# Kernel optimization log

Hardware: AMD Instinct MI355X
Metric: run time of the kernel (lower is better)

The kernel has to match this reference:

```python
import jax, jax.numpy as jnp
import numpy as np

H = 512      # hidden_dim
K = 3        # conv_kernel_size
CHUNK = 3    # chunk_size
EPS = 1e-5   # BatchNorm eps


def conv1d(x, w, b, pad):
    # x: (B, Cin, L), w: (Cout, Cin, K)
    y = jax.lax.conv_general_dilated(x, w, (1,), [(pad, pad)],
                                     dimension_numbers=("NCH", "OIH", "NCH"))
    return y + b[None, :, None]


def chunk_indices(seq_lens):
    # static int metadata -> numpy index build (loop over small fixed batch only)
    sl = np.asarray(seq_lens)
    bidx, sidx = [], []
    for b, l in enumerate(sl):
        starts = np.arange(0, int(l) - CHUNK + 1, CHUNK)
        bidx.append(np.full(starts.shape[0], b, dtype=np.int32))
        sidx.append(starts.astype(np.int32))
    return np.concatenate(bidx), np.concatenate(sidx)


def setup_inputs() -> dict:
    key = jax.random.key(0)
    ks = jax.random.split(key, 8)
    B, L = 32, 4096
    x = jax.random.normal(ks[0], (B, L), jnp.float32)
    seq_lens = jax.random.randint(ks[1], (B,), 2048, L + 1)

    def w(k, shape):
        return jax.random.normal(k, shape, jnp.float32) * 0.05

    return {
        "x": x,
        "w0": w(ks[2], (H, 1, K)), "b0": jnp.zeros((H,)), "g0": jnp.ones((H,)), "be0": jnp.zeros((H,)),
        "w1": w(ks[3], (H, H, K)), "b1": jnp.zeros((H,)), "g1": jnp.ones((H,)), "be1": jnp.zeros((H,)),
        "w2": w(ks[4], (H, H, K)), "b2": jnp.zeros((H,)), "g2": jnp.ones((H,)), "be2": jnp.zeros((H,)),
        "pw": w(ks[5], (H, H, CHUNK)), "pb": jnp.zeros((H,)),
        "fw": w(ks[6], (1, H)), "fb": jnp.zeros((1,)),
        "seq_lens": seq_lens,
    }


def reference(x, w0, b0, g0, be0, w1, b1, g1, be1, w2, b2, g2, be2,
              pw, pb, fw, fb, seq_lens):
    inv = np.float32(1.0 / np.sqrt(1.0 + EPS))  # BN eval: mean=0, var=1
    h = x[:, None, :]  # (B, 1, L)
    for (w, b, g, be) in ((w0, b0, g0, be0), (w1, b1, g1, be1), (w2, b2, g2, be2)):
        h = jax.nn.relu(conv1d(h, w, b, pad=1))
        h = (g * inv)[None, :, None] * h + be[None, :, None]
    h = jnp.transpose(h, (0, 2, 1))  # (B, L, H)

    bidx_np, sidx_np = chunk_indices(seq_lens)
    bidx = jnp.asarray(bidx_np)
    sidx = jnp.asarray(sidx_np)
    offs = jnp.arange(CHUNK, dtype=jnp.int32)
    chunks = h[bidx[:, None], sidx[:, None] + offs[None, :], :]  # (N, CHUNK, H)

    # pre_fc_conv over a length-CHUNK window == one GEMM per chunk
    z = jnp.einsum("nth,cht->nc", chunks, pw) + pb  # (N, H)
    logits = jax.nn.relu(z) @ fw.T + fb             # (N, 1)
    return jax.nn.sigmoid(logits)[:, 0]             # (N,)
```

## Files before the change

### kernel.cpp

```cpp
#include <hip/hip_runtime.h>

#define HCH 512
#define LSEQ 4096
#define HSTR (LSEQ + 4)
#define NB 32
#define KW 3
#define KDIM 1536
#define SPAD 1408
#define INVS 0.9999950000374997f
#define NT 24

typedef __attribute__((ext_vector_type(8))) short bf16x8;
typedef __attribute__((ext_vector_type(4))) float f32x4;

__device__ inline unsigned short f2bf(float f) {
  unsigned int u = __float_as_uint(f);
  u += 0x7fffu + ((u >> 16) & 1u);
  return (unsigned short)(u >> 16);
}

__device__ inline void gl_lds16(const void* g, void* l) {
  __builtin_amdgcn_global_load_lds(
      (const __attribute__((address_space(1))) void*)g,
      (__attribute__((address_space(3))) void*)l, 16, 0, 0);
}

__global__ void prep_all(const float* __restrict__ w1, const float* __restrict__ w2,
                         const float* __restrict__ pw, unsigned short* __restrict__ wt,
                         const int* __restrict__ seq_lens, int* __restrict__ cum,
                         float* __restrict__ pz, int nz,
                         unsigned short* __restrict__ hbuf, int nbp) {
  int idx = blockIdx.x * 256 + threadIdx.x;
  if (idx < nz) pz[idx] = 0.f;
  if (idx == 0) {
    int acc = 0;
    for (int b = 0; b < NB; b++) {
      cum[b] = acc;
      acc += (seq_lens[b] - KW) / KW + 1;
    }
  }
  int npads = 2 * nbp * 4 * HCH;
  if (idx < npads) {
    int per = nbp * 4 * HCH;
    int buf = idx / per, r = idx % per;
    int b = r / (4 * HCH), rr = r % (4 * HCH);
    int j = rr / HCH, c = rr % HCH;
    int row = (j == 0) ? 0 : (LSEQ + j);
    hbuf[((size_t)buf * nbp + b) * HSTR * HCH + (size_t)row * HCH + c] = 0;
  }
  if (idx < 3 * HCH * KDIM) {
    int which = idx / (HCH * KDIM);
    int r = idx % (HCH * KDIM);
    int c = r / KDIM;
    int rem = r % KDIM;
    int k = rem / HCH, ci = rem % HCH;
    const float* src = (which == 0) ? w1 : ((which == 1) ? w2 : pw);
    wt[idx] = f2bf(src[c * KDIM + ci * KW + k]);
  }
}

__global__ void layer0(const float* __restrict__ x, const float* __restrict__ w0,
                       const float* __restrict__ b0, const float* __restrict__ g0,
                       const float* __restrict__ be0, unsigned short* __restrict__ h0,
                       const int* __restrict__ seq_q) {
  int tid = threadIdx.x;
  int wave = tid >> 6, lane = tid & 63;
  int pos0 = (blockIdx.x * 4 + wave) * 8;
  int l0 = pos0 & (LSEQ - 1);
  int bq = pos0 >> 12;
  if (l0 >= seq_q[bq] + 2) return;
  int c0 = lane * 8;

  float w[24], bb[8], gg[8], ee[8];
  for (int v = 0; v < 6; v++)
    *reinterpret_cast<float4*>(w + v * 4) = *reinterpret_cast<const float4*>(w0 + c0 * 3 + v * 4);
  for (int v = 0; v < 2; v++) {
    *reinterpret_cast<float4*>(bb + v * 4) = *reinterpret_cast<const float4*>(b0 + c0 + v * 4);
    *reinterpret_cast<float4*>(gg + v * 4) = *reinterpret_cast<const float4*>(g0 + c0 + v * 4);
    *reinterpret_cast<float4*>(ee + v * 4) = *reinterpret_cast<const float4*>(be0 + c0 + v * 4);
  }
  for (int c = 0; c < 8; c++) gg[c] *= INVS;

  const float* xb = x + (size_t)(pos0 - l0);
  unsigned short* hrow = h0 + ((size_t)bq * HSTR + 1 + l0) * HCH + c0;
  for (int pp = 0; pp < 8; pp++) {
    int l = l0 + pp;
    float xm1 = (l > 0) ? xb[l - 1] : 0.f;
    float xc = xb[l];
    float xp1 = (l < LSEQ - 1) ? xb[l + 1] : 0.f;
    unsigned int o[4];
    for (int pq = 0; pq < 4; pq++) {
      unsigned int lo = 0, hi = 0;
      for (int s = 0; s < 2; s++) {
        int c = pq * 2 + s;
        float y = w[c * 3] * xm1 + w[c * 3 + 1] * xc + w[c * 3 + 2] * xp1 + bb[c];
        y = fmaxf(y, 0.f);
        unsigned int u = f2bf(gg[c] * y + ee[c]);
        if (s == 0) lo = u; else hi = u;
      }
      o[pq] = lo | (hi << 16);
    }
    uint4 v4; v4.x = o[0]; v4.y = o[1]; v4.z = o[2]; v4.w = o[3];
    *reinterpret_cast<uint4*>(hrow + (size_t)pp * HCH) = v4;
  }
}

#define OFFK(T) (((T) % 3) * HCH + ((T) / 3) * 64)

#define STAGE_A(Mh, AB, TN)                                                 \
  { char* d_ = ldsc + (AB) * 32768 + (Mh) * 16384 + w * 1024;               \
    gl_lds16(aSrc[Mh][0] + OFFK(TN), d_);                                   \
    gl_lds16(aSrc[Mh][1] + OFFK(TN), d_ + 8192); }

#define STAGE_B(Nh, BB, TN)                                                 \
  { char* d_ = ldsc + 65536 + (BB) * 32768 + (Nh) * 16384 + w * 1024;       \
    gl_lds16(bSrc[Nh][0] + OFFK(TN), d_);                                   \
    gl_lds16(bSrc[Nh][1] + OFFK(TN), d_ + 8192); }

#define LOAD_AF(Mh, AB)                                                     \
  _Pragma("unroll") for (int i_ = 0; i_ < 4; ++i_)                          \
  _Pragma("unroll") for (int s_ = 0; s_ < 2; ++s_)                          \
    af[i_][s_] = *reinterpret_cast<const bf16x8*>(                          \
        ldsb + (AB) * 16384 + (Mh) * 8192 + (wm + i_ * 16 + mr) * 64 +      \
        (((s_ * 4 + quad) ^ (mr & 7)) << 3));

#define LOAD_BF(Nh, BB)                                                     \
  _Pragma("unroll") for (int j_ = 0; j_ < 2; ++j_)                          \
  _Pragma("unroll") for (int s_ = 0; s_ < 2; ++s_)                          \
    bfv[Nh][j_][s_] = *reinterpret_cast<const bf16x8*>(                     \
        ldsb + 32768 + (BB) * 16384 + (Nh) * 8192 + (wn + j_ * 16 + mr) * 64 + \
        (((s_ * 4 + quad) ^ (mr & 7)) << 3));

#define MFMA_Q(Mh, Nh)                                                      \
  __builtin_amdgcn_s_setprio(1);                                            \
  _Pragma("unroll") for (int i_ = 0; i_ < 4; ++i_)                          \
  _Pragma("unroll") for (int j_ = 0; j_ < 2; ++j_)                          \
  _Pragma("unroll") for (int s_ = 0; s_ < 2; ++s_)                          \
    acc[(Mh)*4 + i_][(Nh)*2 + j_] = __builtin_amdgcn_mfma_f32_16x16x32_bf16( \
        af[i_][s_], bfv[Nh][j_][s_], acc[(Mh)*4 + i_][(Nh)*2 + j_], 0, 0, 0); \
  __builtin_amdgcn_s_setprio(0);

#define BARRIER { asm volatile("" ::: "memory");                            \
                  __builtin_amdgcn_s_barrier();                             \
                  asm volatile("" ::: "memory"); }
#define WAITV(n) asm volatile("s_waitcnt vmcnt(" #n ")" ::: "memory");

#define STEP(T)                                                             \
  {                                                                         \
    if ((T) == NT - 1) { WAITV(0); } else { WAITV(4); }                     \
    BARRIER;                                                                \
    if ((T) + 1 < NT) { STAGE_A(0, ((T)+1)&1, (T)+1);                       \
                        STAGE_A(1, ((T)+1)&1, (T)+1); }                     \
    if ((T) + 2 < NT) { STAGE_B(0, ((T)+2)%3, (T)+2);                       \
                        STAGE_B(1, ((T)+2)%3, (T)+2); }                     \
    bf16x8 af[4][2], bfv[2][2][2];                                          \
    LOAD_AF(0, (T)&1);                                                      \
    LOAD_BF(0, (T)%3); LOAD_BF(1, (T)%3);                                   \
    MFMA_Q(0, 0); MFMA_Q(0, 1);                                             \
    LOAD_AF(1, (T)&1);                                                      \
    MFMA_Q(1, 1); MFMA_Q(1, 0);                                             \
  }

__global__ __launch_bounds__(512, 2) void conv_gemm8(
    const unsigned short* __restrict__ hin,
    const unsigned short* __restrict__ wT,
    const float* __restrict__ bconv, const float* __restrict__ g,
    const float* __restrict__ be,
    unsigned short* __restrict__ hout,
    const int* __restrict__ seq_q, int margin) {
  __shared__ unsigned short ldsb[81920];

  int f = blockIdx.x;
  int cpx = gridDim.x >> 3;
  int s = (f & 7) * cpx + (f >> 3);
  int cm = (s & 1) << 8;
  int y = s >> 1;
  int b = y >> 4;
  int l0 = (y & 15) << 8;
  int limit = seq_q[b] + margin;
  if (l0 >= limit) return;

  const size_t hb = (size_t)b * HSTR * HCH + HCH;
  int tid = threadIdx.x;
  int w = tid >> 6, lane = tid & 63;
  int quad = lane >> 4, mr = lane & 15;
  int wm = (w >> 2) << 6;
  int wn = (w & 3) << 5;
  int srow = tid >> 3;
  int sslot8 = (((tid & 7) ^ (srow & 7)) << 3);

  const unsigned short* aSrc[2][2];
#pragma unroll
  for (int Mh = 0; Mh < 2; ++Mh)
#pragma unroll
    for (int g2 = 0; g2 < 2; ++g2)
      aSrc[Mh][g2] = wT + (size_t)(cm + Mh * 128 + g2 * 64 + srow) * KDIM + sslot8;
  const unsigned short* bSrc[2][2];
#pragma unroll
  for (int Nh = 0; Nh < 2; ++Nh)
#pragma unroll
    for (int g2 = 0; g2 < 2; ++g2)
      bSrc[Nh][g2] = hin + hb +
          (size_t)(l0 - 1 + Nh * 128 + g2 * 64 + srow) * HCH + sslot8;

  f32x4 acc[8][4] = {};
  char* ldsc = (char*)ldsb;

  STAGE_A(0, 0, 0); STAGE_A(1, 0, 0);
  STAGE_B(0, 0, 0); STAGE_B(1, 0, 0);
  STAGE_B(0, 1, 1); STAGE_B(1, 1, 1);

  STEP(0)  STEP(1)  STEP(2)  STEP(3)  STEP(4)  STEP(5)
  STEP(6)  STEP(7)  STEP(8)  STEP(9)  STEP(10) STEP(11)
  STEP(12) STEP(13) STEP(14) STEP(15) STEP(16) STEP(17)
  STEP(18) STEP(19) STEP(20) STEP(21) STEP(22) STEP(23)

#pragma unroll
  for (int ai = 0; ai < 8; ++ai) {
    int Mh = ai >> 2, i = ai & 3;
    int c = cm + Mh * 128 + wm + i * 16 + quad * 4;
    f32x4 bc = *reinterpret_cast<const f32x4*>(bconv + c);
    f32x4 gg = *reinterpret_cast<const f32x4*>(g + c);
    f32x4 bb = *reinterpret_cast<const f32x4*>(be + c);
#pragma unroll
    for (int aj = 0; aj < 4; ++aj) {
      int Nh = aj >> 1, j = aj & 1;
      int n = l0 + Nh * 128 + wn + j * 16 + (lane & 15);
      if (n >= limit) continue;
      unsigned long long pack = 0;
#pragma unroll
      for (int r = 0; r < 4; ++r) {
        float yv = acc[ai][aj][r] + bc[r];
        yv = fmaxf(yv, 0.f);
        unsigned long long u = f2bf(gg[r] * INVS * yv + bb[r]);
        pack |= u << (16 * r);
      }
      *reinterpret_cast<unsigned long long*>(hout + hb + (size_t)n * HCH + c) = pack;
    }
  }
}

__global__ __launch_bounds__(256) void chunk_gemm(
    const unsigned short* __restrict__ h2,
    const unsigned short* __restrict__ wTp,
    const float* __restrict__ pb, const float* __restrict__ fw,
    const int* __restrict__ seq_q,
    const int* __restrict__ cum_q,
    float* __restrict__ partial,
    const unsigned short* __restrict__ zp) {
  __shared__ unsigned short As[3 * 128 * 32];
  __shared__ unsigned short Bs[384 * 32];

  int tid = threadIdx.x;
  int wave = tid >> 6, lane = tid & 63;
  int cm = blockIdx.x * 128;
  int b = blockIdx.y / (SPAD / 128);
  int s_base = (blockIdx.y % (SPAD / 128)) * 128;
  int slen = seq_q[b];
  if (3 * s_base + KW > slen) return;
  int p_base = 3 * s_base;
  int wm = (wave >> 1) * 64;
  int wn = (wave & 1) * 64;
  const size_t hb = (size_t)b * HSTR * HCH + HCH;

  f32x4 acc[4][4] = {};

  int lr = lane >> 2, lc = (lane & 3) * 8;

  const unsigned short* bptr[6];
  const unsigned short* aptr[6];
  unsigned aoff[6];
  for (int t = 0; t < 6; t++) {
    int c = wave * 6 + t;
    int p = p_base + c * 16 + lr;
    bptr[t] = (p < LSEQ) ? (h2 + hb + (size_t)p * HCH + lc) : (zp + lc);
    int k = c >> 3, c8 = c & 7;
    aptr[t] = wTp + (size_t)(cm + c8 * 16 + lr) * KDIM + k * HCH + lc;
    aoff[t] = (unsigned)(k * 4096 + c8 * 512) * 2;
  }

  for (int it = 0; it < 16; it++) {
    int ci0 = it * 32;
    for (int t = 0; t < 6; t++) {
      gl_lds16(aptr[t] + ci0, (char*)As + aoff[t]);
      gl_lds16(bptr[t] + ci0, (char*)Bs + (wave * 6 + t) * 1024);
    }
    __syncthreads();

    int quad = lane >> 4, mr = lane & 15;
    for (int t = 0; t < 3; t++) {
      bf16x8 af[4], bfr[4];
      for (int i = 0; i < 4; i++)
        af[i] = *reinterpret_cast<const bf16x8*>(As + t * 4096 + (wm + i * 16 + mr) * 32 + quad * 8);
      for (int j = 0; j < 4; j++)
        bfr[j] = *reinterpret_cast<const bf16x8*>(Bs + (3 * (wn + j * 16 + mr) + t) * 32 + quad * 8);
      for (int i = 0; i < 4; i++)
        for (int j = 0; j < 4; j++)
          acc[i][j] = __builtin_amdgcn_mfma_f32_16x16x32_bf16(af[i], bfr[j], acc[i][j], 0, 0, 0);
    }
    __syncthreads();
  }

  int quad = lane >> 4, nn = lane & 15;
  for (int j = 0; j < 4; j++) {
    float s = 0.f;
    for (int i = 0; i < 4; i++) {
      int c = cm + wm + i * 16 + quad * 4;
      f32x4 pbv = *reinterpret_cast<const f32x4*>(pb + c);
      f32x4 fwv = *reinterpret_cast<const f32x4*>(fw + c);
      for (int r = 0; r < 4; r++) {
        float z = acc[i][j][r] + pbv[r];
        z = fmaxf(z, 0.f);
        s += z * fwv[r];
      }
    }
    s += __shfl_xor(s, 16, 64);
    s += __shfl_xor(s, 32, 64);
    if (quad == 0) {
      int sc = s_base + wn + j * 16 + nn;
      if (3 * sc + KW <= slen) atomicAdd(partial + cum_q[b] + sc, s);
    }
  }
}

__global__ void finalize(const float* __restrict__ partial, const float* __restrict__ fb,
                         float* __restrict__ out, int n) {
  int i = blockIdx.x * 256 + threadIdx.x;
  if (i < n) {
    float t = partial[i] + fb[0];
    out[i] = 1.f / (1.f + expf(-t));
  }
}

extern "C" void kernel_launch(void* const* d_in, const int* in_sizes, int n_in,
                              void* d_out, int out_size, void* d_ws, size_t ws_size,
                              hipStream_t stream) {
  (void)in_sizes; (void)n_in;
  const float* x   = (const float*)d_in[0];
  const float* w0  = (const float*)d_in[1];
  const float* b0  = (const float*)d_in[2];
  const float* g0  = (const float*)d_in[3];
  const float* be0 = (const float*)d_in[4];
  const float* w1  = (const float*)d_in[5];
  const float* b1  = (const float*)d_in[6];
  const float* g1  = (const float*)d_in[7];
  const float* be1 = (const float*)d_in[8];
  const float* w2  = (const float*)d_in[9];
  const float* b2  = (const float*)d_in[10];
  const float* g2  = (const float*)d_in[11];
  const float* be2 = (const float*)d_in[12];
  const float* pw  = (const float*)d_in[13];
  const float* pb  = (const float*)d_in[14];
  const float* fw  = (const float*)d_in[15];
  const float* fb  = (const float*)d_in[16];
  const int* seq_lens = (const int*)d_in[17];

  char* ws = (char*)d_ws;
  unsigned short* zeropage = (unsigned short*)ws;
  float* partial = (float*)(ws + 4096);
  size_t off = 4096 + (size_t)out_size * 4;
  off = (off + 255) & ~(size_t)255;
  int* cum = (int*)(ws + off);
  off += NB * 4;
  off = (off + 255) & ~(size_t)255;
  unsigned short* wt = (unsigned short*)(ws + off);
  off += (size_t)3 * HCH * KDIM * 2;
  off = (off + 255) & ~(size_t)255;
  size_t fixed = off;

  const size_t per_batch = (size_t)HSTR * HCH * 2;
  int nb_pass = NB;
  while (nb_pass > 1 && fixed + 2 * per_batch * (size_t)nb_pass > ws_size)
    nb_pass >>= 1;
  unsigned short* h0 = (unsigned short*)(ws + fixed);
  unsigned short* h1 = h0 + (size_t)nb_pass * HSTR * HCH;

  int nzero = 1024 + out_size;
  prep_all<<<(3 * HCH * KDIM) / 256, 256, 0, stream>>>(w1, w2, pw, wt, seq_lens, cum,
                                                       (float*)ws, nzero, h0, nb_pass);

  int npass = NB / nb_pass;
  for (int q = 0; q < npass; q++) {
    const float* xq = x + (size_t)q * nb_pass * LSEQ;
    const int* sq = seq_lens + q * nb_pass;
    int nwg = nb_pass * 32;
    layer0<<<nb_pass * (LSEQ / 32), 256, 0, stream>>>(xq, w0, b0, g0, be0, h0, sq);
    conv_gemm8<<<nwg, 512, 0, stream>>>(h0, wt, b1, g1, be1, h1, sq, 1);
    conv_gemm8<<<nwg, 512, 0, stream>>>(h1, wt + (size_t)HCH * KDIM, b2, g2, be2, h0,
                                        sq, 0);
    chunk_gemm<<<dim3(4, nb_pass * (SPAD / 128)), 256, 0, stream>>>(
        h0, wt + (size_t)2 * HCH * KDIM, pb, fw,
        sq, cum + q * nb_pass, partial, zeropage);
  }
  finalize<<<(out_size + 255) / 256, 256, 0, stream>>>(partial, fb, (float*)d_out, out_size);
}
```

Before: 599.4 us.

## Interleave LDS fragment loads, async staging and MFMA clusters with fine-grained barriers

```diff
diff --git a/kernel.cpp b/kernel.cpp
--- a/kernel.cpp
+++ b/kernel.cpp
@@ -131,13 +131,13 @@
         ldsb + 32768 + (BB) * 16384 + (Nh) * 8192 + (wn + j_ * 16 + mr) * 64 + \
         (((s_ * 4 + quad) ^ (mr & 7)) << 3));
 
-#define MFMA_Q(Mh, Nh)                                                      \
+#define MFMA_Q(MB, Nh)                                                      \
   __builtin_amdgcn_s_setprio(1);                                            \
   _Pragma("unroll") for (int i_ = 0; i_ < 4; ++i_)                          \
   _Pragma("unroll") for (int j_ = 0; j_ < 2; ++j_)                          \
   _Pragma("unroll") for (int s_ = 0; s_ < 2; ++s_)                          \
-    acc[(Mh)*4 + i_][(Nh)*2 + j_] = __builtin_amdgcn_mfma_f32_16x16x32_bf16( \
-        af[i_][s_], bfv[Nh][j_][s_], acc[(Mh)*4 + i_][(Nh)*2 + j_], 0, 0, 0); \
+    acc[(MB) + i_][(Nh)*2 + j_] = __builtin_amdgcn_mfma_f32_16x16x32_bf16(  \
+        af[i_][s_], bfv[Nh][j_][s_], acc[(MB) + i_][(Nh)*2 + j_], 0, 0, 0); \
   __builtin_amdgcn_s_setprio(0);
 
 #define BARRIER { asm volatile("" ::: "memory");                            \
@@ -147,18 +147,33 @@
 
 #define STEP(T)                                                             \
   {                                                                         \
-    if ((T) == NT - 1) { WAITV(0); } else { WAITV(4); }                     \
-    BARRIER;                                                                \
-    if ((T) + 1 < NT) { STAGE_A(0, ((T)+1)&1, (T)+1);                       \
-                        STAGE_A(1, ((T)+1)&1, (T)+1); }                     \
-    if ((T) + 2 < NT) { STAGE_B(0, ((T)+2)%3, (T)+2);                       \
-                        STAGE_B(1, ((T)+2)%3, (T)+2); }                     \
-    bf16x8 af[4][2], bfv[2][2][2];                                          \
-    LOAD_AF(0, (T)&1);                                                      \
-    LOAD_BF(0, (T)%3); LOAD_BF(1, (T)%3);                                   \
-    MFMA_Q(0, 0); MFMA_Q(0, 1);                                             \
-    LOAD_AF(1, (T)&1);                                                      \
-    MFMA_Q(1, 1); MFMA_Q(1, 0);                                             \
+                                                 \
+    LOAD_AF(0, (T) & 1);                                                    \
+    LOAD_BF(0, (T) % 3);                                                    \
+    if ((T) + 1 < NT) STAGE_A(0, ((T) + 1) & 1, (T) + 1);                   \
+    BARRIER;                                                                \
+    MFMA_Q(0, 0);                                                           \
+    BARRIER;                                                                \
+                                                 \
+    LOAD_BF(1, (T) % 3);                                                    \
+    if ((T) + 1 < NT) STAGE_A(1, ((T) + 1) & 1, (T) + 1);                   \
+    BARRIER;                                                                \
+    MFMA_Q(0, 1);                                                           \
+    BARRIER;                                                                \
+                       \
+    LOAD_AF(1, (T) & 1);                                                    \
+    if ((T) + 2 < NT) STAGE_B(0, ((T) + 2) % 3, (T) + 2);                   \
+    BARRIER;                                                                \
+    MFMA_Q(4, 1);                                                           \
+    BARRIER;                                                                \
+                                                 \
+    if ((T) + 2 < NT) STAGE_B(1, ((T) + 2) % 3, (T) + 2);                   \
+    BARRIER;                                                                \
+    MFMA_Q(4, 0);                                                           \
+    if ((T) < NT - 1) {                                                     \
+      if ((T) + 2 < NT) { WAITV(4); } else { WAITV(0); }                    \
+      BARRIER;                                                              \
+    }                                                                       \
   }
 
 __global__ __launch_bounds__(512, 2) void conv_gemm8(
@@ -205,10 +220,13 @@
 
   f32x4 acc[8][4] = {};
   char* ldsc = (char*)ldsb;
+  bf16x8 af[4][2], bfv[2][2][2];
 
   STAGE_A(0, 0, 0); STAGE_A(1, 0, 0);
   STAGE_B(0, 0, 0); STAGE_B(1, 0, 0);
   STAGE_B(0, 1, 1); STAGE_B(1, 1, 1);
+  WAITV(4);
+  BARRIER;
 
   STEP(0)  STEP(1)  STEP(2)  STEP(3)  STEP(4)  STEP(5)
   STEP(6)  STEP(7)  STEP(8)  STEP(9)  STEP(10) STEP(11)
```

After: 604.2 us. No clear change (+0.8%).

## Fuse layer0 conv into first conv GEMM, generating B panels in LDS

Applied to the files above, without the earlier changes.

```diff
diff --git a/kernel.cpp b/kernel.cpp
--- a/kernel.cpp
+++ b/kernel.cpp
@@ -59,63 +59,12 @@
   }
 }
 
-__global__ void layer0(const float* __restrict__ x, const float* __restrict__ w0,
-                       const float* __restrict__ b0, const float* __restrict__ g0,
-                       const float* __restrict__ be0, unsigned short* __restrict__ h0,
-                       const int* __restrict__ seq_q) {
-  int tid = threadIdx.x;
-  int wave = tid >> 6, lane = tid & 63;
-  int pos0 = (blockIdx.x * 4 + wave) * 8;
-  int l0 = pos0 & (LSEQ - 1);
-  int bq = pos0 >> 12;
-  if (l0 >= seq_q[bq] + 2) return;
-  int c0 = lane * 8;
-
-  float w[24], bb[8], gg[8], ee[8];
-  for (int v = 0; v < 6; v++)
-    *reinterpret_cast<float4*>(w + v * 4) = *reinterpret_cast<const float4*>(w0 + c0 * 3 + v * 4);
-  for (int v = 0; v < 2; v++) {
-    *reinterpret_cast<float4*>(bb + v * 4) = *reinterpret_cast<const float4*>(b0 + c0 + v * 4);
-    *reinterpret_cast<float4*>(gg + v * 4) = *reinterpret_cast<const float4*>(g0 + c0 + v * 4);
-    *reinterpret_cast<float4*>(ee + v * 4) = *reinterpret_cast<const float4*>(be0 + c0 + v * 4);
-  }
-  for (int c = 0; c < 8; c++) gg[c] *= INVS;
-
-  const float* xb = x + (size_t)(pos0 - l0);
-  unsigned short* hrow = h0 + ((size_t)bq * HSTR + 1 + l0) * HCH + c0;
-  for (int pp = 0; pp < 8; pp++) {
-    int l = l0 + pp;
-    float xm1 = (l > 0) ? xb[l - 1] : 0.f;
-    float xc = xb[l];
-    float xp1 = (l < LSEQ - 1) ? xb[l + 1] : 0.f;
-    unsigned int o[4];
-    for (int pq = 0; pq < 4; pq++) {
-      unsigned int lo = 0, hi = 0;
-      for (int s = 0; s < 2; s++) {
-        int c = pq * 2 + s;
-        float y = w[c * 3] * xm1 + w[c * 3 + 1] * xc + w[c * 3 + 2] * xp1 + bb[c];
-        y = fmaxf(y, 0.f);
-        unsigned int u = f2bf(gg[c] * y + ee[c]);
-        if (s == 0) lo = u; else hi = u;
-      }
-      o[pq] = lo | (hi << 16);
-    }
-    uint4 v4; v4.x = o[0]; v4.y = o[1]; v4.z = o[2]; v4.w = o[3];
-    *reinterpret_cast<uint4*>(hrow + (size_t)pp * HCH) = v4;
-  }
-}
-
 #define OFFK(T) (((T) % 3) * HCH + ((T) / 3) * 64)
 
 #define STAGE_A(Mh, AB, TN)                                                 \
   { char* d_ = ldsc + (AB) * 32768 + (Mh) * 16384 + w * 1024;               \
     gl_lds16(aSrc[Mh][0] + OFFK(TN), d_);                                   \
     gl_lds16(aSrc[Mh][1] + OFFK(TN), d_ + 8192); }
-
-#define STAGE_B(Nh, BB, TN)                                                 \
-  { char* d_ = ldsc + 65536 + (BB) * 32768 + (Nh) * 16384 + w * 1024;       \
-    gl_lds16(bSrc[Nh][0] + OFFK(TN), d_);                                   \
-    gl_lds16(bSrc[Nh][1] + OFFK(TN), d_ + 8192); }
 
 #define LOAD_AF(Mh, AB)                                                     \
   _Pragma("unroll") for (int i_ = 0; i_ < 4; ++i_)                          \
@@ -124,26 +73,178 @@
         ldsb + (AB) * 16384 + (Mh) * 8192 + (wm + i_ * 16 + mr) * 64 +      \
         (((s_ * 4 + quad) ^ (mr & 7)) << 3));
 
+#define MFMA_Q(MB, Nh)                                                      \
+  __builtin_amdgcn_s_setprio(1);                                            \
+  _Pragma("unroll") for (int i_ = 0; i_ < 4; ++i_)                          \
+  _Pragma("unroll") for (int j_ = 0; j_ < 2; ++j_)                          \
+  _Pragma("unroll") for (int s_ = 0; s_ < 2; ++s_)                          \
+    acc[(MB) + i_][(Nh)*2 + j_] = __builtin_amdgcn_mfma_f32_16x16x32_bf16(  \
+        af[i_][s_], bfv[Nh][j_][s_], acc[(MB) + i_][(Nh)*2 + j_], 0, 0, 0); \
+  __builtin_amdgcn_s_setprio(0);
+
+#define BARRIER { asm volatile("" ::: "memory");                            \
+                  __builtin_amdgcn_s_barrier();                             \
+                  asm volatile("" ::: "memory"); }
+#define WAITV(n) asm volatile("s_waitcnt vmcnt(" #n ")" ::: "memory");
+#define WAITL0   asm volatile("s_waitcnt lgkmcnt(0)" ::: "memory");
+
+#define LOAD_BF_F(Nh, CB, K)                                                \
+  _Pragma("unroll") for (int j_ = 0; j_ < 2; ++j_)                          \
+  _Pragma("unroll") for (int s_ = 0; s_ < 2; ++s_) {                        \
+    int row_ = (Nh) * 128 + wn + j_ * 16 + mr + (K);                        \
+    bfv[Nh][j_][s_] = *reinterpret_cast<const bf16x8*>(                     \
+        ldsb + 32768 + (CB) * 16512 + row_ * 64 +                           \
+        (((s_ * 4 + quad) ^ (row_ & 7)) << 3)); }
+
+#define PANEL(CB, CI0)                                                      \
+  { float wp0[8], wp1[8], wp2[8], wpb[8], wpg[8], wpe[8];                   \
+    _Pragma("unroll") for (int c8 = 0; c8 < 8; ++c8) {                      \
+      const float* wl_ = flds + 32896 + ((CI0) + c8) * 8;                   \
+      wp0[c8] = wl_[0]; wp1[c8] = wl_[1]; wp2[c8] = wl_[2];                 \
+      wpb[c8] = wl_[3]; wpg[c8] = wl_[4]; wpe[c8] = wl_[5]; }               \
+    _Pragma("unroll") for (int j_ = 0; j_ < 5; ++j_) {                      \
+      if (j_ < 4 || lane < 2) {                                             \
+        int row_ = (j_ < 4) ? (lane + 64 * j_) : (256 + lane);              \
+        int p_ = l0 - 1 + row_;                                             \
+        unsigned ov_[4];                                                    \
+        _Pragma("unroll") for (int q_ = 0; q_ < 4; ++q_) {                  \
+          unsigned lo_ = 0, hi_ = 0;                                        \
+          _Pragma("unroll") for (int s2 = 0; s2 < 2; ++s2) {                \
+            int c8 = q_ * 2 + s2;                                           \
+            float y_ = wp0[c8] * xv[j_][0] + wp1[c8] * xv[j_][1] +          \
+                       wp2[c8] * xv[j_][2] + wpb[c8];                       \
+            y_ = fmaxf(y_, 0.f);                                            \
+            unsigned u_ = f2bf(wpg[c8] * y_ + wpe[c8]);                     \
+            if (s2 == 0) lo_ = u_; else hi_ = u_;                           \
+          }                                                                 \
+          ov_[q_] = lo_ | (hi_ << 16);                                      \
+        }                                                                   \
+        if (p_ < 0 || p_ >= LSEQ) { ov_[0]=0; ov_[1]=0; ov_[2]=0; ov_[3]=0; }\
+        uint4 vv_; vv_.x=ov_[0]; vv_.y=ov_[1]; vv_.z=ov_[2]; vv_.w=ov_[3];  \
+        *reinterpret_cast<uint4*>(ldsc + 65536 + (CB) * 33024 +             \
+            row_ * 128 + ((w ^ (row_ & 7)) << 4)) = vv_;                    \
+      } } }
+
+#define STEPF(T)                                                            \
+  {                                                                         \
+    if ((T) % 3 == 0) { WAITL0; }                                           \
+    WAITV(0);                                                               \
+    BARRIER;                                                                \
+    if ((T) + 1 < NT) { STAGE_A(0, ((T)+1)&1, (T)+1);                       \
+                        STAGE_A(1, ((T)+1)&1, (T)+1); }                     \
+    bf16x8 af[4][2], bfv[2][2][2];                                          \
+    LOAD_AF(0, (T) & 1);                                                    \
+    LOAD_BF_F(0, ((T)/3) & 1, (T) % 3); LOAD_BF_F(1, ((T)/3) & 1, (T) % 3); \
+    MFMA_Q(0, 0); MFMA_Q(0, 1);                                             \
+    LOAD_AF(1, (T) & 1);                                                    \
+    MFMA_Q(4, 1); MFMA_Q(4, 0);                                             \
+    if ((T) % 3 == 2 && (T)/3 + 1 < 8) PANEL(((T)/3 + 1) & 1,               \
+                                             ((T)/3 + 1) * 64 + w * 8);     \
+  }
+
+__global__ __launch_bounds__(512, 2) void conv_gemm_f(
+    const float* __restrict__ x,
+    const unsigned short* __restrict__ wT,
+    const float* __restrict__ bconv, const float* __restrict__ g,
+    const float* __restrict__ be,
+    unsigned short* __restrict__ hout,
+    const int* __restrict__ seq_q,
+    const float* __restrict__ w0, const float* __restrict__ b0,
+    const float* __restrict__ g0, const float* __restrict__ be0) {
+  __shared__ unsigned short ldsb[73984];
+
+  int f = blockIdx.x;
+  int cpx = gridDim.x >> 3;
+  int s = (f & 7) * cpx + (f >> 3);
+  int cm = (s & 1) << 8;
+  int y = s >> 1;
+  int b = y >> 4;
+  int l0 = (y & 15) << 8;
+  int limit = seq_q[b] + 1;
+  if (l0 >= limit) return;
+
+  const size_t hb = (size_t)b * HSTR * HCH + HCH;
+  int tid = threadIdx.x;
+  int w = tid >> 6, lane = tid & 63;
+  int quad = lane >> 4, mr = lane & 15;
+  int wm = (w >> 2) << 6;
+  int wn = (w & 3) << 5;
+  int srow = tid >> 3;
+  int sslot8 = (((tid & 7) ^ (srow & 7)) << 3);
+
+  const unsigned short* aSrc[2][2];
+#pragma unroll
+  for (int Mh = 0; Mh < 2; ++Mh)
+#pragma unroll
+    for (int g2 = 0; g2 < 2; ++g2)
+      aSrc[Mh][g2] = wT + (size_t)(cm + Mh * 128 + g2 * 64 + srow) * KDIM + sslot8;
+
+  f32x4 acc[8][4] = {};
+  char* ldsc = (char*)ldsb;
+  float* flds = reinterpret_cast<float*>(ldsb);
+  const float* xk = x + (size_t)b * LSEQ;
+
+  float xv[5][3];
+#pragma unroll
+  for (int j = 0; j < 5; ++j) {
+    int row = (j < 4) ? (lane + 64 * j) : (256 + lane);
+    bool on = (j < 4) || (lane < 2);
+#pragma unroll
+    for (int d = 0; d < 3; ++d) {
+      int idx = l0 - 2 + row + d;
+      xv[j][d] = (on && idx >= 0 && idx < LSEQ) ? xk[idx] : 0.f;
+    }
+  }
+  {
+    float* wl = flds + 32896 + tid * 8;
+    wl[0] = w0[3 * tid]; wl[1] = w0[3 * tid + 1]; wl[2] = w0[3 * tid + 2];
+    wl[3] = b0[tid]; wl[4] = g0[tid] * INVS; wl[5] = be0[tid];
+  }
+  __syncthreads();
+  PANEL(0, w * 8);
+  STAGE_A(0, 0, 0); STAGE_A(1, 0, 0);
+
+  STEPF(0)  STEPF(1)  STEPF(2)  STEPF(3)  STEPF(4)  STEPF(5)
+  STEPF(6)  STEPF(7)  STEPF(8)  STEPF(9)  STEPF(10) STEPF(11)
+  STEPF(12) STEPF(13) STEPF(14) STEPF(15) STEPF(16) STEPF(17)
+  STEPF(18) STEPF(19) STEPF(20) STEPF(21) STEPF(22) STEPF(23)
+
+#pragma unroll
+  for (int ai = 0; ai < 8; ++ai) {
+    int Mh = ai >> 2, i = ai & 3;
+    int c = cm + Mh * 128 + wm + i * 16 + quad * 4;
+    f32x4 bc = *reinterpret_cast<const f32x4*>(bconv + c);
+    f32x4 gg = *reinterpret_cast<const f32x4*>(g + c);
+    f32x4 bb = *reinterpret_cast<const f32x4*>(be + c);
+#pragma unroll
+    for (int aj = 0; aj < 4; ++aj) {
+      int Nh = aj >> 1, j = aj & 1;
+      int n = l0 + Nh * 128 + wn + j * 16 + (lane & 15);
+      if (n >= limit) continue;
+      unsigned long long pack = 0;
+#pragma unroll
+      for (int r = 0; r < 4; ++r) {
+        float yv = acc[ai][aj][r] + bc[r];
+        yv = fmaxf(yv, 0.f);
+        unsigned long long u = f2bf(gg[r] * INVS * yv + bb[r]);
+        pack |= u << (16 * r);
+      }
+      *reinterpret_cast<unsigned long long*>(hout + hb + (size_t)n * HCH + c) = pack;
+    }
+  }
+}
+
+#define STAGE_B(Nh, BB, TN)                                                 \
+  { char* d_ = ldsc + 65536 + (BB) * 32768 + (Nh) * 16384 + w * 1024;       \
+    gl_lds16(bSrc[Nh][0] + OFFK(TN), d_);                                   \
+    gl_lds16(bSrc[Nh][1] + OFFK(TN), d_ + 8192); }
+
 #define LOAD_BF(Nh, BB)                                                     \
   _Pragma("unroll") for (int j_ = 0; j_ < 2; ++j_)                          \
   _Pragma("unroll") for (int s_ = 0; s_ < 2; ++s_)                          \
     bfv[Nh][j_][s_] = *reinterpret_cast<const bf16x8*>(                     \
         ldsb + 32768 + (BB) * 16384 + (Nh) * 8192 + (wn + j_ * 16 + mr) * 64 + \
         (((s_ * 4 + quad) ^ (mr & 7)) << 3));
-
-#define MFMA_Q(Mh, Nh)                                                      \
-  __builtin_amdgcn_s_setprio(1);                                            \
-  _Pragma("unroll") for (int i_ = 0; i_ < 4; ++i_)                          \
-  _Pragma("unroll") for (int j_ = 0; j_ < 2; ++j_)                          \
-  _Pragma("unroll") for (int s_ = 0; s_ < 2; ++s_)                          \
-    acc[(Mh)*4 + i_][(Nh)*2 + j_] = __builtin_amdgcn_mfma_f32_16x16x32_bf16( \
-        af[i_][s_], bfv[Nh][j_][s_], acc[(Mh)*4 + i_][(Nh)*2 + j_], 0, 0, 0); \
-  __builtin_amdgcn_s_setprio(0);
-
-#define BARRIER { asm volatile("" ::: "memory");                            \
-                  __builtin_amdgcn_s_barrier();                             \
-                  asm volatile("" ::: "memory"); }
-#define WAITV(n) asm volatile("s_waitcnt vmcnt(" #n ")" ::: "memory");
 
 #define STEP(T)                                                             \
   {                                                                         \
@@ -158,7 +259,7 @@
     LOAD_BF(0, (T)%3); LOAD_BF(1, (T)%3);                                   \
     MFMA_Q(0, 0); MFMA_Q(0, 1);                                             \
     LOAD_AF(1, (T)&1);                                                      \
-    MFMA_Q(1, 1); MFMA_Q(1, 0);                                             \
+    MFMA_Q(4, 1); MFMA_Q(4, 0);                                             \
   }
 
 __global__ __launch_bounds__(512, 2) void conv_gemm8(
@@ -384,8 +485,8 @@
     const float* xq = x + (size_t)q * nb_pass * LSEQ;
     const int* sq = seq_lens + q * nb_pass;
     int nwg = nb_pass * 32;
-    layer0<<<nb_pass * (LSEQ / 32), 256, 0, stream>>>(xq, w0, b0, g0, be0, h0, sq);
-    conv_gemm8<<<nwg, 512, 0, stream>>>(h0, wt, b1, g1, be1, h1, sq, 1);
+    conv_gemm_f<<<nwg, 512, 0, stream>>>(xq, wt, b1, g1, be1, h1, sq,
+                                         w0, b0, g0, be0);
     conv_gemm8<<<nwg, 512, 0, stream>>>(h1, wt + (size_t)HCH * KDIM, b2, g2, be2, h0,
                                         sq, 0);
     chunk_gemm<<<dim3(4, nb_pass * (SPAD / 128)), 256, 0, stream>>>(
```

Result: slower. 678.7 us (+13.2%).

## Rewrite chunk GEMM to reuse pipelined 256x256 conv GEMM tile machinery

Applied to the files above, without the earlier changes.

```diff
diff --git a/kernel.cpp b/kernel.cpp
--- a/kernel.cpp
+++ b/kernel.cpp
@@ -6,7 +6,6 @@
 #define NB 32
 #define KW 3
 #define KDIM 1536
-#define SPAD 1408
 #define INVS 0.9999950000374997f
 #define NT 24
 
@@ -131,13 +130,13 @@
         ldsb + 32768 + (BB) * 16384 + (Nh) * 8192 + (wn + j_ * 16 + mr) * 64 + \
         (((s_ * 4 + quad) ^ (mr & 7)) << 3));
 
-#define MFMA_Q(Mh, Nh)                                                      \
+#define MFMA_Q(MB, Nh)                                                      \
   __builtin_amdgcn_s_setprio(1);                                            \
   _Pragma("unroll") for (int i_ = 0; i_ < 4; ++i_)                          \
   _Pragma("unroll") for (int j_ = 0; j_ < 2; ++j_)                          \
   _Pragma("unroll") for (int s_ = 0; s_ < 2; ++s_)                          \
-    acc[(Mh)*4 + i_][(Nh)*2 + j_] = __builtin_amdgcn_mfma_f32_16x16x32_bf16( \
-        af[i_][s_], bfv[Nh][j_][s_], acc[(Mh)*4 + i_][(Nh)*2 + j_], 0, 0, 0); \
+    acc[(MB) + i_][(Nh)*2 + j_] = __builtin_amdgcn_mfma_f32_16x16x32_bf16(  \
+        af[i_][s_], bfv[Nh][j_][s_], acc[(MB) + i_][(Nh)*2 + j_], 0, 0, 0); \
   __builtin_amdgcn_s_setprio(0);
 
 #define BARRIER { asm volatile("" ::: "memory");                            \
@@ -158,7 +157,7 @@
     LOAD_BF(0, (T)%3); LOAD_BF(1, (T)%3);                                   \
     MFMA_Q(0, 0); MFMA_Q(0, 1);                                             \
     LOAD_AF(1, (T)&1);                                                      \
-    MFMA_Q(1, 1); MFMA_Q(1, 0);                                             \
+    MFMA_Q(4, 1); MFMA_Q(4, 0);                                             \
   }
 
 __global__ __launch_bounds__(512, 2) void conv_gemm8(
@@ -240,86 +239,87 @@
   }
 }
 
-__global__ __launch_bounds__(256) void chunk_gemm(
+__global__ __launch_bounds__(512, 2) void chunk_gemm8(
     const unsigned short* __restrict__ h2,
-    const unsigned short* __restrict__ wTp,
+    const unsigned short* __restrict__ wT,
     const float* __restrict__ pb, const float* __restrict__ fw,
     const int* __restrict__ seq_q,
     const int* __restrict__ cum_q,
     float* __restrict__ partial,
     const unsigned short* __restrict__ zp) {
-  __shared__ unsigned short As[3 * 128 * 32];
-  __shared__ unsigned short Bs[384 * 32];
-
-  int tid = threadIdx.x;
-  int wave = tid >> 6, lane = tid & 63;
-  int cm = blockIdx.x * 128;
-  int b = blockIdx.y / (SPAD / 128);
-  int s_base = (blockIdx.y % (SPAD / 128)) * 128;
+  __shared__ unsigned short ldsb[81920];
+
+  int f = blockIdx.x;
+  int cpx = gridDim.x >> 3;
+  int s = (f & 7) * cpx + (f >> 3);
+  int cm = (s & 1) << 8;
+  int y = s >> 1;
+  int b = y / 6;
+  int s_base = (y % 6) << 8;
   int slen = seq_q[b];
   if (3 * s_base + KW > slen) return;
-  int p_base = 3 * s_base;
-  int wm = (wave >> 1) * 64;
-  int wn = (wave & 1) * 64;
+
   const size_t hb = (size_t)b * HSTR * HCH + HCH;
-
-  f32x4 acc[4][4] = {};
-
-  int lr = lane >> 2, lc = (lane & 3) * 8;
-
-  const unsigned short* bptr[6];
-  const unsigned short* aptr[6];
-  unsigned aoff[6];
-  for (int t = 0; t < 6; t++) {
-    int c = wave * 6 + t;
-    int p = p_base + c * 16 + lr;
-    bptr[t] = (p < LSEQ) ? (h2 + hb + (size_t)p * HCH + lc) : (zp + lc);
-    int k = c >> 3, c8 = c & 7;
-    aptr[t] = wTp + (size_t)(cm + c8 * 16 + lr) * KDIM + k * HCH + lc;
-    aoff[t] = (unsigned)(k * 4096 + c8 * 512) * 2;
-  }
-
-  for (int it = 0; it < 16; it++) {
-    int ci0 = it * 32;
-    for (int t = 0; t < 6; t++) {
-      gl_lds16(aptr[t] + ci0, (char*)As + aoff[t]);
-      gl_lds16(bptr[t] + ci0, (char*)Bs + (wave * 6 + t) * 1024);
-    }
-    __syncthreads();
-
-    int quad = lane >> 4, mr = lane & 15;
-    for (int t = 0; t < 3; t++) {
-      bf16x8 af[4], bfr[4];
-      for (int i = 0; i < 4; i++)
-        af[i] = *reinterpret_cast<const bf16x8*>(As + t * 4096 + (wm + i * 16 + mr) * 32 + quad * 8);
-      for (int j = 0; j < 4; j++)
-        bfr[j] = *reinterpret_cast<const bf16x8*>(Bs + (3 * (wn + j * 16 + mr) + t) * 32 + quad * 8);
-      for (int i = 0; i < 4; i++)
-        for (int j = 0; j < 4; j++)
-          acc[i][j] = __builtin_amdgcn_mfma_f32_16x16x32_bf16(af[i], bfr[j], acc[i][j], 0, 0, 0);
-    }
-    __syncthreads();
-  }
-
-  int quad = lane >> 4, nn = lane & 15;
-  for (int j = 0; j < 4; j++) {
-    float s = 0.f;
-    for (int i = 0; i < 4; i++) {
-      int c = cm + wm + i * 16 + quad * 4;
+  int tid = threadIdx.x;
+  int w = tid >> 6, lane = tid & 63;
+  int quad = lane >> 4, mr = lane & 15;
+  int wm = (w >> 2) << 6;
+  int wn = (w & 3) << 5;
+  int srow = tid >> 3;
+  int sslot8 = (((tid & 7) ^ (srow & 7)) << 3);
+
+  const unsigned short* aSrc[2][2];
+#pragma unroll
+  for (int Mh = 0; Mh < 2; ++Mh)
+#pragma unroll
+    for (int g2 = 0; g2 < 2; ++g2)
+      aSrc[Mh][g2] = wT + (size_t)(cm + Mh * 128 + g2 * 64 + srow) * KDIM + sslot8;
+  const unsigned short* bSrc[2][2];
+#pragma unroll
+  for (int Nh = 0; Nh < 2; ++Nh)
+#pragma unroll
+    for (int g2 = 0; g2 < 2; ++g2) {
+      int slot = s_base + Nh * 128 + g2 * 64 + srow;
+      bSrc[Nh][g2] = (slot <= 1365)
+          ? h2 + hb + (size_t)(3 * slot) * HCH + sslot8
+          : zp + sslot8;
+    }
+
+  f32x4 acc[8][4] = {};
+  char* ldsc = (char*)ldsb;
+
+  STAGE_A(0, 0, 0); STAGE_A(1, 0, 0);
+  STAGE_B(0, 0, 0); STAGE_B(1, 0, 0);
+  STAGE_B(0, 1, 1); STAGE_B(1, 1, 1);
+
+  STEP(0)  STEP(1)  STEP(2)  STEP(3)  STEP(4)  STEP(5)
+  STEP(6)  STEP(7)  STEP(8)  STEP(9)  STEP(10) STEP(11)
+  STEP(12) STEP(13) STEP(14) STEP(15) STEP(16) STEP(17)
+  STEP(18) STEP(19) STEP(20) STEP(21) STEP(22) STEP(23)
+
+  int nn = lane & 15;
+#pragma unroll
+  for (int aj = 0; aj < 4; ++aj) {
+    int Nh = aj >> 1, jj = aj & 1;
+    int sc = s_base + Nh * 128 + wn + jj * 16 + nn;
+    float sacc = 0.f;
+#pragma unroll
+    for (int ai = 0; ai < 8; ++ai) {
+      int Mh = ai >> 2, i = ai & 3;
+      int c = cm + Mh * 128 + wm + i * 16 + quad * 4;
       f32x4 pbv = *reinterpret_cast<const f32x4*>(pb + c);
       f32x4 fwv = *reinterpret_cast<const f32x4*>(fw + c);
-      for (int r = 0; r < 4; r++) {
-        float z = acc[i][j][r] + pbv[r];
+#pragma unroll
+      for (int r = 0; r < 4; ++r) {
+        float z = acc[ai][aj][r] + pbv[r];
         z = fmaxf(z, 0.f);
-        s += z * fwv[r];
+        sacc += z * fwv[r];
       }
     }
-    s += __shfl_xor(s, 16, 64);
-    s += __shfl_xor(s, 32, 64);
-    if (quad == 0) {
-      int sc = s_base + wn + j * 16 + nn;
-      if (3 * sc + KW <= slen) atomicAdd(partial + cum_q[b] + sc, s);
-    }
+    sacc += __shfl_xor(sacc, 16, 64);
+    sacc += __shfl_xor(sacc, 32, 64);
+    if (quad == 0 && 3 * sc + KW <= slen)
+      atomicAdd(partial + cum_q[b] + sc, sacc);
   }
 }
 
@@ -388,9 +388,9 @@
     conv_gemm8<<<nwg, 512, 0, stream>>>(h0, wt, b1, g1, be1, h1, sq, 1);
     conv_gemm8<<<nwg, 512, 0, stream>>>(h1, wt + (size_t)HCH * KDIM, b2, g2, be2, h0,
                                         sq, 0);
-    chunk_gemm<<<dim3(4, nb_pass * (SPAD / 128)), 256, 0, stream>>>(
-        h0, wt + (size_t)2 * HCH * KDIM, pb, fw,
-        sq, cum + q * nb_pass, partial, zeropage);
+    int nwg2 = nb_pass * 12;
+    chunk_gemm8<<<nwg2, 512, 0, stream>>>(h0, wt + (size_t)2 * HCH * KDIM, pb, fw,
+                                          sq, cum + q * nb_pass, partial, zeropage);
   }
   finalize<<<(out_size + 255) / 256, 256, 0, stream>>>(partial, fb, (float*)d_out, out_size);
 }
```

After: 556.4 us (median of 3 runs). -7.2%, faster.
